# Optimization experiments

Hardware: AMD Instinct MI355X
Metric: run time of the kernel (lower is better)

Reference implementation:

```python
import jax, jax.numpy as jnp
import numpy as np

TAU_PRE = 2.0   # pre-synaptic trace time constant
SCALE = 1.0     # forward(scale=1.0) default
SPIKE_P = 0.1   # firing probability for realistic binary spike trains


def setup_inputs() -> dict:
    key = jax.random.key(0)
    k1, k2 = jax.random.split(key)
    T, B, NIN, NOUT = 2048, 128, 256, 128
    # binary spike trains, [T, B, N]
    in_spikes = (jax.random.uniform(k1, (T, B, NIN)) < SPIKE_P).astype(jnp.float32)
    out_spikes = (jax.random.uniform(k2, (T, B, NOUT)) < SPIKE_P).astype(jnp.float32)
    return {"in_spikes": in_spikes, "out_spikes": out_spikes}


def reference(in_spikes, out_spikes):
    # STDP.forward: loop over recorded timesteps, per step:
    #   trace_pre = trace_pre - trace_pre/tau_pre + in_spike          (decayed trace)
    #   dw = sum_b trace_pre[b, :] (outer) out_spike[b, :] -> [NOUT, NIN]
    #   delta_w += scale * dw
    # Expressed as a single lax.scan over the time axis.
    B, NIN = in_spikes.shape[1], in_spikes.shape[2]
    NOUT = out_spikes.shape[2]

    def step(carry, xs):
        trace_pre, delta_w = carry
        s_in, s_out = xs                                 # [B, NIN], [B, NOUT]
        trace_pre = trace_pre - trace_pre / TAU_PRE + s_in
        dw = jnp.einsum('bi,bo->oi', trace_pre, s_out)   # [NOUT, NIN]
        return (trace_pre, delta_w + SCALE * dw), None

    init = (jnp.zeros((B, NIN), in_spikes.dtype),
            jnp.zeros((NOUT, NIN), in_spikes.dtype))
    (_, delta_w), _ = jax.lax.scan(step, init, (in_spikes, out_spikes))
    return delta_w
```

## Files before the change

kernel.cpp:

```cpp
#include <hip/hip_runtime.h>
#include <hip/hip_bf16.h>

#define T_TOTAL 2048
#define BATCH   128
#define NIN     256
#define NOUT    128

#define TC      256
#define BC      4
#define WARM    32
#define G       4
#define NTC     (T_TOTAL / TC)
#define NBC     (BATCH / BC)
#define NBLOCKS (NTC * NBC)
#define NG      (TC / G)

#define ROWU      24
#define OUT_ELEMS (NOUT * NIN)

typedef __attribute__((ext_vector_type(8)))  __bf16 bf16x8;
typedef __attribute__((ext_vector_type(2)))  __bf16 bf16x2;
typedef __attribute__((ext_vector_type(16))) float  f32x16;

static __device__ __forceinline__ unsigned pack_bf16(float a, float b) {
    bf16x2 v = { (__bf16)a, (__bf16)b };
    union { bf16x2 v; unsigned u; } c; c.v = v; return c.u;
}

__global__ __launch_bounds__(512, 2)
void stdp_main(const float* __restrict__ in, const float* __restrict__ outs,
               float* __restrict__ dst, int nslots, int use_atomic)
{
    __shared__ unsigned short tr_lds[2][NIN * ROWU];
    __shared__ unsigned short ot_lds[2][NOUT * ROWU];

    const int tid = threadIdx.x;
    const int bc  = blockIdx.x % NBC;
    const int tc  = blockIdx.x / NBC;
    const int b0  = bc * BC;
    const int t0  = tc * TC;

    const int i_idx = tid & 255;
    const int bh    = tid >> 8;
    const int o_idx = tid & 127;
    const int blo   = (tid >> 7) & 3;

    float tr0 = 0.f, tr1 = 0.f;

    if (tc > 0) {
        for (int t = t0 - WARM; t < t0; t += 8) {
            float v0[8], v1[8];
#pragma unroll
            for (int u = 0; u < 8; ++u) {
                const size_t base = ((size_t)(t + u) * BATCH + b0 + 2 * bh) * NIN + i_idx;
                v0[u] = in[base];
                v1[u] = in[base + NIN];
            }
#pragma unroll
            for (int u = 0; u < 8; ++u) {
                tr0 = 0.5f * tr0 + v0[u];
                tr1 = 0.5f * tr1 + v1[u];
            }
        }
    }

    f32x16 acc[4];
#pragma unroll
    for (int j = 0; j < 4; ++j) acc[j] = (f32x16)(0.f);

    const int lane  = tid & 63;
    const int wv    = tid >> 6;
    const int mt    = wv & 3;
    const int ntb   = (wv >> 2) * 4;
    const int l31   = lane & 31;
    const int khalf = lane >> 5;

    float P0[2][G], P1[2][G], PO[2][G];

    auto load_stage = [&](int s, int g) {
        const int tg = t0 + g * G;
#pragma unroll
        for (int q = 0; q < G; ++q) {
            const size_t baseI = ((size_t)(tg + q) * BATCH + b0 + 2 * bh) * NIN + i_idx;
            P0[s][q] = in[baseI];
            P1[s][q] = in[baseI + NIN];
            PO[s][q] = outs[((size_t)(tg + q) * BATCH + b0 + blo) * NOUT + o_idx];
        }
    };

    auto body = [&](int s, int g) {
        unsigned words[G];
        __bf16 ob[G];
#pragma unroll
        for (int q = 0; q < G; ++q) {
            tr0 = 0.5f * tr0 + P0[s][q];
            tr1 = 0.5f * tr1 + P1[s][q];
            words[q] = pack_bf16(tr0, tr1);
            ob[q] = (__bf16)PO[s][q];
        }
        if (g + 2 < NG) load_stage(s, g + 2);

        unsigned* trow = (unsigned*)&tr_lds[s][i_idx * ROWU];
#pragma unroll
        for (int q = 0; q < G; ++q) trow[q * 2 + bh] = words[q];
        __bf16* orow = (__bf16*)&ot_lds[s][o_idx * ROWU];
#pragma unroll
        for (int q = 0; q < G; ++q) orow[q * 4 + blo] = ob[q];

        __syncthreads();

        const bf16x8 a = *(const bf16x8*)&ot_lds[s][(mt * 32 + l31) * ROWU + khalf * 8];
#pragma unroll
        for (int j = 0; j < 4; ++j) {
            const bf16x8 b = *(const bf16x8*)&tr_lds[s][((ntb + j) * 32 + l31) * ROWU + khalf * 8];
            acc[j] = __builtin_amdgcn_mfma_f32_32x32x16_bf16(a, b, acc[j], 0, 0, 0);
        }
    };

    load_stage(0, 0);
    load_stage(1, 1);
    for (int gg = 0; gg < NG; gg += 2) {
        body(0, gg);
        body(1, gg + 1);
    }

    float* base = dst + (size_t)(use_atomic ? (blockIdx.x % nslots) : blockIdx.x) * OUT_ELEMS;
#pragma unroll
    for (int j = 0; j < 4; ++j) {
        const int icol = (ntb + j) * 32 + l31;
#pragma unroll
        for (int r = 0; r < 16; ++r) {
            const int row = (r & 3) + 8 * (r >> 2) + 4 * khalf;
            const int o   = mt * 32 + row;
            const float v = acc[j][r];
            if (use_atomic) atomicAdd(&base[o * NIN + icol], v);
            else            base[o * NIN + icol] = v;
        }
    }
}

__global__ void zero_kernel(float* p, int n) {
    int i = blockIdx.x * blockDim.x + threadIdx.x;
    if (i < n) p[i] = 0.f;
}

__global__ __launch_bounds__(256)
void reduce_kernel(const float* __restrict__ ws, float* __restrict__ outp, int nslots) {
    const int idx = blockIdx.x * 256 + threadIdx.x;
    float s = 0.f;
    int k = 0;
    for (; k + 16 <= nslots; k += 16) {
        float v[16];
#pragma unroll
        for (int u = 0; u < 16; ++u) v[u] = ws[(size_t)(k + u) * OUT_ELEMS + idx];
#pragma unroll
        for (int u = 0; u < 16; ++u) s += v[u];
    }
    for (; k < nslots; ++k) s += ws[(size_t)k * OUT_ELEMS + idx];
    outp[idx] = s;
}

extern "C" void kernel_launch(void* const* d_in, const int* in_sizes, int n_in,
                              void* d_out, int out_size, void* d_ws, size_t ws_size,
                              hipStream_t stream) {
    const float* in   = (const float*)d_in[0];
    const float* outs = (const float*)d_in[1];
    float* out = (float*)d_out;
    float* ws  = (float*)d_ws;

    const size_t slot_bytes = (size_t)OUT_ELEMS * sizeof(float);

    if (ws_size >= (size_t)NBLOCKS * slot_bytes) {
        stdp_main<<<NBLOCKS, 512, 0, stream>>>(in, outs, ws, NBLOCKS, 0);
        reduce_kernel<<<OUT_ELEMS / 256, 256, 0, stream>>>(ws, out, NBLOCKS);
    } else if (ws_size >= 16 * slot_bytes) {
        zero_kernel<<<(16 * OUT_ELEMS + 255) / 256, 256, 0, stream>>>(ws, 16 * OUT_ELEMS);
        stdp_main<<<NBLOCKS, 512, 0, stream>>>(in, outs, ws, 16, 1);
        reduce_kernel<<<OUT_ELEMS / 256, 256, 0, stream>>>(ws, out, 16);
    } else {
        zero_kernel<<<(OUT_ELEMS + 255) / 256, 256, 0, stream>>>(out, OUT_ELEMS);
        stdp_main<<<NBLOCKS, 512, 0, stream>>>(in, outs, out, 1, 1);
    }
}
```

Baseline: 452.1 us.

## Vectorize spike loads, swizzle LDS layout, halve time chunk for more blocks

Each thread now loads float2 pairs of adjacent input/output neurons instead of scalar loads across batch rows, and the staged trace/output tiles are written to LDS with an XOR swizzle on the k-offset so the MFMA operand reads and the packed writes avoid bank conflicts. The time chunk is halved, doubling the block count, and the launch bound is raised to four blocks per CU for more parallelism. The cost is twice as many warm-up recomputations and twice as many partial slots to reduce, plus tighter register limits.

```diff
diff --git a/kernel.cpp b/kernel.cpp
--- a/kernel.cpp
+++ b/kernel.cpp
@@ -6,7 +6,7 @@
 #define NIN     256
 #define NOUT    128
 
-#define TC      256
+#define TC      128
 #define BC      4
 #define WARM    32
 #define G       4
@@ -16,7 +16,10 @@
 #define NG      (TC / G)
 
 #define ROWU      24
+#define ROWD      12
 #define OUT_ELEMS (NOUT * NIN)
+
+static_assert(NG % 2 == 0, "pipeline needs even group count");
 
 typedef __attribute__((ext_vector_type(8)))  __bf16 bf16x8;
 typedef __attribute__((ext_vector_type(2)))  __bf16 bf16x2;
@@ -27,7 +30,7 @@
     union { bf16x2 v; unsigned u; } c; c.v = v; return c.u;
 }
 
-__global__ __launch_bounds__(512, 2)
+__global__ __launch_bounds__(512, 4)
 void stdp_main(const float* __restrict__ in, const float* __restrict__ outs,
                float* __restrict__ dst, int nslots, int use_atomic)
 {
@@ -40,26 +43,30 @@
     const int b0  = bc * BC;
     const int t0  = tc * TC;
 
-    const int i_idx = tid & 255;
-    const int bh    = tid >> 8;
-    const int o_idx = tid & 127;
-    const int blo   = (tid >> 7) & 3;
+    const int i0  = (tid & 127) * 2;
+    const int btr = (tid >> 7) & 3;
+    const int o0  = (tid & 63) * 2;
+    const int bo  = (tid >> 6) & 3;
+    const int q2  = (tid >> 8) & 1;
+
+    const float2* __restrict__ inp  =
+        (const float2*)(in + (size_t)(b0 + btr) * NIN + i0);
+    const float2* __restrict__ outp =
+        (const float2*)(outs + (size_t)(b0 + bo) * NOUT + o0);
+    const size_t IST = (size_t)BATCH * NIN  / 2;
+    const size_t OST = (size_t)BATCH * NOUT / 2;
 
     float tr0 = 0.f, tr1 = 0.f;
 
     if (tc > 0) {
         for (int t = t0 - WARM; t < t0; t += 8) {
-            float v0[8], v1[8];
+            float2 v[8];
+#pragma unroll
+            for (int u = 0; u < 8; ++u) v[u] = inp[(size_t)(t + u) * IST];
 #pragma unroll
             for (int u = 0; u < 8; ++u) {
-                const size_t base = ((size_t)(t + u) * BATCH + b0 + 2 * bh) * NIN + i_idx;
-                v0[u] = in[base];
-                v1[u] = in[base + NIN];
-            }
-#pragma unroll
-            for (int u = 0; u < 8; ++u) {
-                tr0 = 0.5f * tr0 + v0[u];
-                tr1 = 0.5f * tr1 + v1[u];
+                tr0 = 0.5f * tr0 + v[u].x;
+                tr1 = 0.5f * tr1 + v[u].y;
             }
         }
     }
@@ -75,44 +82,62 @@
     const int l31   = lane & 31;
     const int khalf = lane >> 5;
 
-    float P0[2][G], P1[2][G], PO[2][G];
+    const int vtr  = (i0 >> 5) & 1;
+    const int vot  = (o0 >> 5) & 1;
+    const int kb   = btr * 2;
+    const int ko   = bo * 2 + q2;
+    const int trw0 = i0 * ROWD + ((kb)     ^ (vtr << 2));
+    const int trw1 = i0 * ROWD + ((kb + 1) ^ (vtr << 2));
+    const int otw0 = o0 * ROWD + ((ko)     ^ (vot << 2));
+
+    const int ard = (mt * 32 + l31) * ROWU + ((khalf ^ (mt & 1)) << 3);
+    const int brd0 = l31 * ROWU;
+
+    float2 PI[2][G];
+    float2 PO[2][2];
 
     auto load_stage = [&](int s, int g) {
         const int tg = t0 + g * G;
 #pragma unroll
+        for (int q = 0; q < G; ++q) PI[s][q] = inp[(size_t)(tg + q) * IST];
+#pragma unroll
+        for (int u = 0; u < 2; ++u) PO[s][u] = outp[(size_t)(tg + 2 * q2 + u) * OST];
+    };
+
+    auto body = [&](int s, int g) {
+        float a0[G], a1[G];
+#pragma unroll
         for (int q = 0; q < G; ++q) {
-            const size_t baseI = ((size_t)(tg + q) * BATCH + b0 + 2 * bh) * NIN + i_idx;
-            P0[s][q] = in[baseI];
-            P1[s][q] = in[baseI + NIN];
-            PO[s][q] = outs[((size_t)(tg + q) * BATCH + b0 + blo) * NOUT + o_idx];
-        }
-    };
-
-    auto body = [&](int s, int g) {
-        unsigned words[G];
-        __bf16 ob[G];
-#pragma unroll
-        for (int q = 0; q < G; ++q) {
-            tr0 = 0.5f * tr0 + P0[s][q];
-            tr1 = 0.5f * tr1 + P1[s][q];
-            words[q] = pack_bf16(tr0, tr1);
-            ob[q] = (__bf16)PO[s][q];
-        }
+            tr0 = 0.5f * tr0 + PI[s][q].x;
+            tr1 = 0.5f * tr1 + PI[s][q].y;
+            a0[q] = tr0; a1[q] = tr1;
+        }
+        const unsigned w00 = pack_bf16(a0[0], a0[1]);
+        const unsigned w01 = pack_bf16(a0[2], a0[3]);
+        const unsigned w10 = pack_bf16(a1[0], a1[1]);
+        const unsigned w11 = pack_bf16(a1[2], a1[3]);
+        const unsigned wo0 = pack_bf16(PO[s][0].x, PO[s][1].x);
+        const unsigned wo1 = pack_bf16(PO[s][0].y, PO[s][1].y);
+
         if (g + 2 < NG) load_stage(s, g + 2);
 
-        unsigned* trow = (unsigned*)&tr_lds[s][i_idx * ROWU];
-#pragma unroll
-        for (int q = 0; q < G; ++q) trow[q * 2 + bh] = words[q];
-        __bf16* orow = (__bf16*)&ot_lds[s][o_idx * ROWU];
-#pragma unroll
-        for (int q = 0; q < G; ++q) orow[q * 4 + blo] = ob[q];
+        unsigned* trl = (unsigned*)&tr_lds[s][0];
+        unsigned* otl = (unsigned*)&ot_lds[s][0];
+        trl[trw0]        = w00;
+        trl[trw1]        = w01;
+        trl[trw0 + ROWD] = w10;
+        trl[trw1 + ROWD] = w11;
+        otl[otw0]        = wo0;
+        otl[otw0 + ROWD] = wo1;
 
         __syncthreads();
 
-        const bf16x8 a = *(const bf16x8*)&ot_lds[s][(mt * 32 + l31) * ROWU + khalf * 8];
+        const bf16x8 a = *(const bf16x8*)&ot_lds[s][ard];
 #pragma unroll
         for (int j = 0; j < 4; ++j) {
-            const bf16x8 b = *(const bf16x8*)&tr_lds[s][((ntb + j) * 32 + l31) * ROWU + khalf * 8];
+            const int bn = ntb + j;
+            const bf16x8 b = *(const bf16x8*)
+                &tr_lds[s][bn * (32 * ROWU) + brd0 + ((khalf ^ (bn & 1)) << 3)];
             acc[j] = __builtin_amdgcn_mfma_f32_32x32x16_bf16(a, b, acc[j], 0, 0, 0);
         }
     };
```

Result: slower. 478.0 us (+5.7%).

## Reformulate STDP as reverse-time post-trace recurrence and drop LDS staging

Applied to the files above, without the earlier changes.

Uses the identity sum_t trace_pre(t)·out(t) = sum_t in(t)·rtrace_post(t) to run a backward-in-time trace over the output spikes. Each wave then builds its MFMA A/B fragments directly from registers loaded from global memory, with no LDS round trip and no __syncthreads. The warm-up now reads future output timesteps instead of past input timesteps. This removes the LDS transpose and the per-group barrier, at the cost of more per-thread global loads, since each wave now loads its own input slices, and higher register pressure.

```diff
diff --git a/kernel.cpp b/kernel.cpp
--- a/kernel.cpp
+++ b/kernel.cpp
@@ -15,8 +15,9 @@
 #define NBLOCKS (NTC * NBC)
 #define NG      (TC / G)
 
-#define ROWU      24
 #define OUT_ELEMS (NOUT * NIN)
+
+static_assert(NG % 2 == 0, "2-stage pipeline needs even group count");
 
 typedef __attribute__((ext_vector_type(8)))  __bf16 bf16x8;
 typedef __attribute__((ext_vector_type(2)))  __bf16 bf16x2;
@@ -27,39 +28,49 @@
     union { bf16x2 v; unsigned u; } c; c.v = v; return c.u;
 }
 
+static __device__ __forceinline__ bf16x8 frag_from4(unsigned d0, unsigned d1,
+                                                    unsigned d2, unsigned d3) {
+    union { unsigned u[4]; bf16x8 v; } c;
+    c.u[0] = d0; c.u[1] = d1; c.u[2] = d2; c.u[3] = d3; return c.v;
+}
+
 __global__ __launch_bounds__(512, 2)
 void stdp_main(const float* __restrict__ in, const float* __restrict__ outs,
                float* __restrict__ dst, int nslots, int use_atomic)
 {
-    __shared__ unsigned short tr_lds[2][NIN * ROWU];
-    __shared__ unsigned short ot_lds[2][NOUT * ROWU];
-
     const int tid = threadIdx.x;
     const int bc  = blockIdx.x % NBC;
     const int tc  = blockIdx.x / NBC;
     const int b0  = bc * BC;
     const int t0  = tc * TC;
 
-    const int i_idx = tid & 255;
-    const int bh    = tid >> 8;
-    const int o_idx = tid & 127;
-    const int blo   = (tid >> 7) & 3;
+    const int lane = tid & 63;
+    const int wv   = tid >> 6;
+    const int mt   = wv & 3;
+    const int nh   = wv >> 2;
+    const int l31  = lane & 31;
+    const int kh   = lane >> 5;
 
-    float tr0 = 0.f, tr1 = 0.f;
+    const size_t IST = (size_t)BATCH * NIN;
+    const size_t OST = (size_t)BATCH * NOUT;
 
-    if (tc > 0) {
-        for (int t = t0 - WARM; t < t0; t += 8) {
-            float v0[8], v1[8];
+    const float* __restrict__ inW  = in   + (size_t)(b0 + 2 * kh) * NIN  + nh * 128 + l31;
+    const float* __restrict__ outW = outs + (size_t)(b0 + 2 * kh) * NOUT + mt * 32  + l31;
+
+    float rtrA = 0.f, rtrB = 0.f;
+
+    if (tc < NTC - 1) {
+        for (int tb = t0 + TC + WARM; tb > t0 + TC; tb -= 8) {
+            float vA[8], vB[8];
 #pragma unroll
             for (int u = 0; u < 8; ++u) {
-                const size_t base = ((size_t)(t + u) * BATCH + b0 + 2 * bh) * NIN + i_idx;
-                v0[u] = in[base];
-                v1[u] = in[base + NIN];
+                vA[u] = outW[(size_t)(tb - 1 - u) * OST];
+                vB[u] = outW[(size_t)(tb - 1 - u) * OST + NOUT];
             }
 #pragma unroll
             for (int u = 0; u < 8; ++u) {
-                tr0 = 0.5f * tr0 + v0[u];
-                tr1 = 0.5f * tr1 + v1[u];
+                rtrA = vA[u] + 0.5f * rtrA;
+                rtrB = vB[u] + 0.5f * rtrB;
             }
         }
     }
@@ -68,69 +79,62 @@
 #pragma unroll
     for (int j = 0; j < 4; ++j) acc[j] = (f32x16)(0.f);
 
-    const int lane  = tid & 63;
-    const int wv    = tid >> 6;
-    const int mt    = wv & 3;
-    const int ntb   = (wv >> 2) * 4;
-    const int l31   = lane & 31;
-    const int khalf = lane >> 5;
-
-    float P0[2][G], P1[2][G], PO[2][G];
+    float AO[2][8];
+    float BI[2][32];
 
     auto load_stage = [&](int s, int g) {
         const int tg = t0 + g * G;
 #pragma unroll
         for (int q = 0; q < G; ++q) {
-            const size_t baseI = ((size_t)(tg + q) * BATCH + b0 + 2 * bh) * NIN + i_idx;
-            P0[s][q] = in[baseI];
-            P1[s][q] = in[baseI + NIN];
-            PO[s][q] = outs[((size_t)(tg + q) * BATCH + b0 + blo) * NOUT + o_idx];
+            AO[s][q]     = outW[(size_t)(tg + q) * OST];
+            AO[s][4 + q] = outW[(size_t)(tg + q) * OST + NOUT];
         }
+#pragma unroll
+        for (int tn = 0; tn < 4; ++tn)
+#pragma unroll
+            for (int be = 0; be < 2; ++be)
+#pragma unroll
+                for (int q = 0; q < G; ++q)
+                    BI[s][tn * 8 + be * 4 + q] =
+                        inW[(size_t)(tg + q) * IST + be * NIN + tn * 32];
     };
 
     auto body = [&](int s, int g) {
-        unsigned words[G];
-        __bf16 ob[G];
+        float aA[4], aB[4];
 #pragma unroll
-        for (int q = 0; q < G; ++q) {
-            tr0 = 0.5f * tr0 + P0[s][q];
-            tr1 = 0.5f * tr1 + P1[s][q];
-            words[q] = pack_bf16(tr0, tr1);
-            ob[q] = (__bf16)PO[s][q];
+        for (int q = 3; q >= 0; --q) {
+            rtrA = AO[s][q]     + 0.5f * rtrA; aA[q] = rtrA;
+            rtrB = AO[s][4 + q] + 0.5f * rtrB; aB[q] = rtrB;
         }
-        if (g + 2 < NG) load_stage(s, g + 2);
-
-        unsigned* trow = (unsigned*)&tr_lds[s][i_idx * ROWU];
+        const bf16x8 a = frag_from4(pack_bf16(aA[0], aA[1]), pack_bf16(aA[2], aA[3]),
+                                    pack_bf16(aB[0], aB[1]), pack_bf16(aB[2], aB[3]));
+        bf16x8 bfr[4];
 #pragma unroll
-        for (int q = 0; q < G; ++q) trow[q * 2 + bh] = words[q];
-        __bf16* orow = (__bf16*)&ot_lds[s][o_idx * ROWU];
+        for (int tn = 0; tn < 4; ++tn) {
+            const float* p = &BI[s][tn * 8];
+            bfr[tn] = frag_from4(pack_bf16(p[0], p[1]), pack_bf16(p[2], p[3]),
+                                 pack_bf16(p[4], p[5]), pack_bf16(p[6], p[7]));
+        }
+        if (g >= 2) load_stage(s, g - 2);
 #pragma unroll
-        for (int q = 0; q < G; ++q) orow[q * 4 + blo] = ob[q];
-
-        __syncthreads();
-
-        const bf16x8 a = *(const bf16x8*)&ot_lds[s][(mt * 32 + l31) * ROWU + khalf * 8];
-#pragma unroll
-        for (int j = 0; j < 4; ++j) {
-            const bf16x8 b = *(const bf16x8*)&tr_lds[s][((ntb + j) * 32 + l31) * ROWU + khalf * 8];
-            acc[j] = __builtin_amdgcn_mfma_f32_32x32x16_bf16(a, b, acc[j], 0, 0, 0);
-        }
+        for (int tn = 0; tn < 4; ++tn)
+            acc[tn] = __builtin_amdgcn_mfma_f32_32x32x16_bf16(a, bfr[tn], acc[tn], 0, 0, 0);
     };
 
-    load_stage(0, 0);
-    load_stage(1, 1);
-    for (int gg = 0; gg < NG; gg += 2) {
-        body(0, gg);
-        body(1, gg + 1);
+    load_stage(1, NG - 1);
+    load_stage(0, NG - 2);
+    for (int gg = NG - 1; gg >= 1; gg -= 2) {
+        body(1, gg);
+        body(0, gg - 1);
     }
 
     float* base = dst + (size_t)(use_atomic ? (blockIdx.x % nslots) : blockIdx.x) * OUT_ELEMS;
 #pragma unroll
     for (int j = 0; j < 4; ++j) {
-        const int icol = (ntb + j) * 32 + l31;
+        const int icol = (nh * 4 + j) * 32 + l31;
 #pragma unroll
         for (int r = 0; r < 16; ++r) {
-            const int row = (r & 3) + 8 * (r >> 2) + 4 * khalf;
+            const int row = (r & 3) + 8 * (r >> 2) + 4 * kh;
             const int o   = mt * 32 + row;
             const float v = acc[j][r];
             if (use_atomic) atomicAdd(&base[o * NIN + icol], v);
```

Result: no change. 453.8 us (+0.4%).
